# Optimization experiments

Measured on AMD Instinct MI355X. Metric: run time of the kernel, lower is better.

Reference implementation:

```python
import jax, jax.numpy as jnp
import numpy as np

NH, DK, DV = 16, 32, 16   # num_heads, d_k, d_v ; NH*DV == 256 (residual constraint)
CIN = 256
B, S = 4, 32
EPS = 1e-6


def setup_inputs() -> dict:
    key = jax.random.key(0)
    ks = jax.random.split(key, 16)
    def w(k, shape, fan_in):
        return jax.random.normal(k, shape, jnp.float32) / np.sqrt(fan_in)
    return {
        "x":  jax.random.normal(ks[0], (B, S, S, S, CIN), jnp.float32),
        "Wq": w(ks[1], (CIN, NH * DK), CIN), "bq": jnp.zeros((NH * DK,), jnp.float32),
        "Wk": w(ks[2], (CIN, NH * DK), CIN), "bk": jnp.zeros((NH * DK,), jnp.float32),
        "Wv": w(ks[3], (CIN, NH * DV), CIN), "bv": jnp.zeros((NH * DV,), jnp.float32),
        "W1": w(ks[4], (NH * DV, 2 * NH * DK), NH * DV), "b1": jnp.zeros((2 * NH * DK,), jnp.float32),
        "Wo": w(ks[5], (2 * NH * DK, NH * DV), 2 * NH * DK), "bo": jnp.zeros((NH * DV,), jnp.float32),
        "Wc": w(ks[6], (CIN, 256), CIN), "bc": jnp.zeros((256,), jnp.float32),
        "gamma": jnp.ones((256,), jnp.float32),
        "beta": jnp.zeros((256,), jnp.float32),
        "mu": jnp.zeros((256,), jnp.float32),
        "var": jnp.ones((256,), jnp.float32),
    }


def reference(x, Wq, bq, Wk, bk, Wv, bv, W1, b1, Wo, bo, Wc, bc, gamma, beta, mu, var):
    # 1x1x1 convs == per-voxel dense projections over the channel axis
    q = x @ Wq + bq                                  # [B,S,S,S,NH*DK]
    k = x @ Wk + bk
    v = x @ Wv + bv
    n = B * S * S * S
    q = q.reshape(n, NH, DK)
    k = k.reshape(n, NH, DK)
    v = v.reshape(n, NH, DV)
    # per-voxel attention among heads: scores [n, NH, NH]
    scores = jnp.einsum('nhd,ngd->nhg', q, k) / jnp.sqrt(jnp.float32(DK))
    attn = jax.nn.softmax(scores, axis=-1)
    attn_out = jnp.einsum('nhg,ngv->nhv', attn, v)   # [n, NH, DV]
    attn_out = attn_out.reshape(B, S, S, S, NH * DV)
    # conv FFN
    inter = jax.nn.relu(attn_out @ W1 + b1)          # [B,S,S,S,2*NH*DK]
    inter = inter @ Wo + bo                          # [B,S,S,S,NH*DV]
    # residual branch: 1x1 conv to 256 channels with relu
    res = jax.nn.relu(x @ Wc + bc)                   # [B,S,S,S,256]
    # inference-mode batchnorm (epsilon=1e-6)
    y = (res + inter - mu) * jax.lax.rsqrt(var + EPS) * gamma + beta
    return y
```

## Files before the change

### kernel.cpp

```cpp
#include <hip/hip_runtime.h>
#include <hip/hip_bf16.h>


typedef __bf16 bf16;
typedef __bf16 bf16x8 __attribute__((ext_vector_type(8)));
typedef float f32x4 __attribute__((ext_vector_type(4)));

#define MFMA(a, b, c) __builtin_amdgcn_mfma_f32_16x16x32_bf16((a), (b), (c), 0, 0, 0)

#define THREADS 512
#define TILE 32

constexpr int CIN = 256, NQK = 512, NV = 256, NI = 1024;

constexpr int CH_WQ = 0;
constexpr int CH_WK = 16384;
constexpr int CH_WV = 32768;
constexpr int CH_W1 = 40960;
constexpr int CH_WO = 73728;
constexpr int CH_WC = 106496;
constexpr int CH_TOT = 114688;

constexpr int L_XF  = 0;
constexpr int L_AOF = 8192;
constexpr int L_C   = 16384;
constexpr int L_QS  = L_C;
constexpr int L_KS  = L_C + 16896;
constexpr int L_VS  = L_C + 33792;
constexpr int L_INTF = L_C;
constexpr int LDS_ELEMS = 16384 + 42496;

__global__ void pack_w(const float* __restrict__ Wq, const float* __restrict__ Wk,
                       const float* __restrict__ Wv, const float* __restrict__ W1,
                       const float* __restrict__ Wo, const float* __restrict__ Wc,
                       bf16* __restrict__ ws) {
    int c = blockIdx.x * 256 + threadIdx.x;
    if (c >= CH_TOT) return;
    const float* W; int N, KT, lc;
    if (c < CH_WK)      { W = Wq; N = 512;  KT = 8;  lc = c - CH_WQ; }
    else if (c < CH_WV) { W = Wk; N = 512;  KT = 8;  lc = c - CH_WK; }
    else if (c < CH_W1) { W = Wv; N = 256;  KT = 8;  lc = c - CH_WV; }
    else if (c < CH_WO) { W = W1; N = 1024; KT = 8;  lc = c - CH_W1; }
    else if (c < CH_WC) { W = Wo; N = 256;  KT = 32; lc = c - CH_WO; }
    else                { W = Wc; N = 256;  KT = 8;  lc = c - CH_WC; }
    int lane = lc & 63, tmp = lc >> 6;
    int kt = tmp % KT, nt = tmp / KT;
    int k0 = kt * 32 + (lane >> 4) * 8;
    int n  = nt * 16 + (lane & 15);
    bf16x8 v;
    #pragma unroll
    for (int j = 0; j < 8; ++j) v[j] = (bf16)W[(size_t)(k0 + j) * N + n];
    *(bf16x8*)(ws + (size_t)c * 8) = v;
}

__device__ __forceinline__ bf16x8 lds_afrag(const bf16* smb, int baseoff, int KT,
                                            int mt, int kt, int lane) {
    return *(const bf16x8*)(smb + baseoff + (((mt * KT + kt) * 64) + lane) * 8);
}

__global__ __launch_bounds__(THREADS)
void msa_mfma(const float* __restrict__ x, const bf16* __restrict__ ws,
              const float* __restrict__ bq, const float* __restrict__ bk,
              const float* __restrict__ bv, const float* __restrict__ b1,
              const float* __restrict__ bo, const float* __restrict__ bc,
              const float* __restrict__ gamma, const float* __restrict__ beta,
              const float* __restrict__ mu, const float* __restrict__ var,
              float* __restrict__ out)
{
    extern __shared__ bf16 smb[];
    const int t = threadIdx.x;
    const int lane = t & 63;
    const int wave = t >> 6;
    const int col = lane & 15;
    const int qd  = lane >> 4;
    const size_t base = (size_t)blockIdx.x * (TILE * CIN);

    #pragma unroll
    for (int c2 = t; c2 < 1024; c2 += THREADS) {
        int lc = c2 & 63, kt = (c2 >> 6) & 7, mt = c2 >> 9;
        int vox = mt * 16 + (lc & 15);
        int k0  = kt * 32 + (lc >> 4) * 8;
        const float* src = x + base + vox * 256 + k0;
        float4 f0 = *(const float4*)src;
        float4 f1 = *(const float4*)(src + 4);
        bf16x8 h;
        h[0] = (bf16)f0.x; h[1] = (bf16)f0.y; h[2] = (bf16)f0.z; h[3] = (bf16)f0.w;
        h[4] = (bf16)f1.x; h[5] = (bf16)f1.y; h[6] = (bf16)f1.z; h[7] = (bf16)f1.w;
        *(bf16x8*)&smb[L_XF + c2 * 8] = h;
    }
    __syncthreads();

    {
        f32x4 acc[10][2];
        #pragma unroll
        for (int i = 0; i < 10; ++i) {
            acc[i][0] = (f32x4){0.f, 0.f, 0.f, 0.f};
            acc[i][1] = (f32x4){0.f, 0.f, 0.f, 0.f};
        }
        const bf16* wbase[10];
        #pragma unroll
        for (int i = 0; i < 10; ++i) {
            int g = wave * 10 + i;
            int ch;
            if (g < 32)      ch = CH_WQ + g * 512;
            else if (g < 64) ch = CH_WK + (g - 32) * 512;
            else             ch = CH_WV + (g - 64) * 512;
            wbase[i] = ws + ((size_t)ch + lane) * 8;
        }
        for (int kt = 0; kt < 8; ++kt) {
            bf16x8 a0 = lds_afrag(smb, L_XF, 8, 0, kt, lane);
            bf16x8 a1 = lds_afrag(smb, L_XF, 8, 1, kt, lane);
            #pragma unroll
            for (int i = 0; i < 10; ++i) {
                bf16x8 b = *(const bf16x8*)(wbase[i] + kt * 512);
                acc[i][0] = MFMA(a0, b, acc[i][0]);
                acc[i][1] = MFMA(a1, b, acc[i][1]);
            }
        }
        #pragma unroll
        for (int i = 0; i < 10; ++i) {
            int g = wave * 10 + i;
            int plane, stride, chan;
            float bias;
            if (g < 32)      { chan = g * 16 + col;        bias = bq[chan]; plane = L_QS; stride = 528; }
            else if (g < 64) { chan = (g - 32) * 16 + col; bias = bk[chan]; plane = L_KS; stride = 528; }
            else             { chan = (g - 64) * 16 + col; bias = bv[chan]; plane = L_VS; stride = 272; }
            #pragma unroll
            for (int mt = 0; mt < 2; ++mt)
                #pragma unroll
                for (int r = 0; r < 4; ++r) {
                    int vox = mt * 16 + qd * 4 + r;
                    smb[plane + vox * stride + chan] = (bf16)(acc[i][mt][r] + bias);
                }
        }
    }
    __syncthreads();

    {
        const int vox = t >> 4, h = t & 15;
        const bf16* qp = smb + L_QS + vox * 528 + h * 32;
        float qf[32];
        #pragma unroll
        for (int d8 = 0; d8 < 4; ++d8) {
            bf16x8 qv = *(const bf16x8*)(qp + d8 * 8);
            #pragma unroll
            for (int j = 0; j < 8; ++j) qf[d8 * 8 + j] = (float)qv[j];
        }
        float sc_[16];
        #pragma unroll
        for (int g = 0; g < 16; ++g) {
            const bf16* kp = smb + L_KS + vox * 528 + g * 32;
            float s = 0.f;
            #pragma unroll
            for (int d8 = 0; d8 < 4; ++d8) {
                bf16x8 kv = *(const bf16x8*)(kp + d8 * 8);
                #pragma unroll
                for (int j = 0; j < 8; ++j) s = fmaf((float)kv[j], qf[d8 * 8 + j], s);
            }
            sc_[g] = s * 0.17677669529663687f;
        }
        float m = sc_[0];
        #pragma unroll
        for (int g = 1; g < 16; ++g) m = fmaxf(m, sc_[g]);
        float sum = 0.f;
        #pragma unroll
        for (int g = 0; g < 16; ++g) { sc_[g] = __expf(sc_[g] - m); sum += sc_[g]; }
        const float inv = 1.f / sum;
        float ao[16];
        #pragma unroll
        for (int j = 0; j < 16; ++j) ao[j] = 0.f;
        #pragma unroll
        for (int g = 0; g < 16; ++g) {
            const float a = sc_[g];
            const bf16* vp = smb + L_VS + vox * 272 + g * 16;
            #pragma unroll
            for (int v8 = 0; v8 < 2; ++v8) {
                bf16x8 vv = *(const bf16x8*)(vp + v8 * 8);
                #pragma unroll
                for (int j = 0; j < 8; ++j)
                    ao[v8 * 8 + j] = fmaf(a, (float)vv[j], ao[v8 * 8 + j]);
            }
        }
        const int mt = vox >> 4, m_ = vox & 15, kt = h >> 1;
        #pragma unroll
        for (int half = 0; half < 2; ++half) {
            int quad = (h & 1) * 2 + half;
            bf16x8 o;
            #pragma unroll
            for (int j = 0; j < 8; ++j) o[j] = (bf16)(ao[half * 8 + j] * inv);
            *(bf16x8*)&smb[L_AOF + (((mt * 8 + kt) * 64) + quad * 16 + m_) * 8] = o;
        }
    }
    __syncthreads();

    {
        f32x4 acc[8][2];
        #pragma unroll
        for (int i = 0; i < 8; ++i) {
            acc[i][0] = (f32x4){0.f, 0.f, 0.f, 0.f};
            acc[i][1] = (f32x4){0.f, 0.f, 0.f, 0.f};
        }
        const int n0 = wave * 8;
        for (int kt = 0; kt < 8; ++kt) {
            bf16x8 a0 = lds_afrag(smb, L_AOF, 8, 0, kt, lane);
            bf16x8 a1 = lds_afrag(smb, L_AOF, 8, 1, kt, lane);
            #pragma unroll
            for (int i = 0; i < 8; ++i) {
                bf16x8 b = *(const bf16x8*)(ws + ((size_t)(CH_W1 + ((n0 + i) * 8 + kt) * 64) + lane) * 8);
                acc[i][0] = MFMA(a0, b, acc[i][0]);
                acc[i][1] = MFMA(a1, b, acc[i][1]);
            }
        }
        __syncthreads();
        #pragma unroll
        for (int i = 0; i < 8; ++i) {
            int c = (n0 + i) * 16 + col;
            float bias = b1[c];
            int kt2 = c >> 5;
            int q2  = (c & 31) >> 3;
            int j2  = c & 7;
            #pragma unroll
            for (int mt = 0; mt < 2; ++mt)
                #pragma unroll
                for (int r = 0; r < 4; ++r) {
                    int m_ = qd * 4 + r;
                    float v = fmaxf(acc[i][mt][r] + bias, 0.f);
                    smb[L_INTF + (((mt * 32 + kt2) * 64) + q2 * 16 + m_) * 8 + j2] = (bf16)v;
                }
        }
    }
    __syncthreads();

    {
        f32x4 accF[2][2], accW[2][2];
        #pragma unroll
        for (int i = 0; i < 2; ++i)
            #pragma unroll
            for (int mt = 0; mt < 2; ++mt) {
                accF[i][mt] = (f32x4){0.f, 0.f, 0.f, 0.f};
                accW[i][mt] = (f32x4){0.f, 0.f, 0.f, 0.f};
            }
        const int n0 = wave * 2;
        for (int kt = 0; kt < 32; ++kt) {
            bf16x8 a0 = lds_afrag(smb, L_INTF, 32, 0, kt, lane);
            bf16x8 a1 = lds_afrag(smb, L_INTF, 32, 1, kt, lane);
            #pragma unroll
            for (int i = 0; i < 2; ++i) {
                bf16x8 b = *(const bf16x8*)(ws + ((size_t)(CH_WO + ((n0 + i) * 32 + kt) * 64) + lane) * 8);
                accF[i][0] = MFMA(a0, b, accF[i][0]);
                accF[i][1] = MFMA(a1, b, accF[i][1]);
            }
        }
        for (int kt = 0; kt < 8; ++kt) {
            bf16x8 a0 = lds_afrag(smb, L_XF, 8, 0, kt, lane);
            bf16x8 a1 = lds_afrag(smb, L_XF, 8, 1, kt, lane);
            #pragma unroll
            for (int i = 0; i < 2; ++i) {
                bf16x8 b = *(const bf16x8*)(ws + ((size_t)(CH_WC + ((n0 + i) * 8 + kt) * 64) + lane) * 8);
                accW[i][0] = MFMA(a0, b, accW[i][0]);
                accW[i][1] = MFMA(a1, b, accW[i][1]);
            }
        }
        #pragma unroll
        for (int i = 0; i < 2; ++i) {
            int c = (n0 + i) * 16 + col;
            float bo_ = bo[c], bc_ = bc[c];
            float scl = gamma[c] * rsqrtf(var[c] + 1e-6f);
            float mu_ = mu[c], be_ = beta[c];
            #pragma unroll
            for (int mt = 0; mt < 2; ++mt)
                #pragma unroll
                for (int r = 0; r < 4; ++r) {
                    int vox = mt * 16 + qd * 4 + r;
                    float res = fmaxf(accW[i][mt][r] + bc_, 0.f);
                    float iv  = accF[i][mt][r] + bo_;
                    out[base + vox * 256 + c] = (res + iv - mu_) * scl + be_;
                }
        }
    }
}

extern "C" void kernel_launch(void* const* d_in, const int* in_sizes, int n_in,
                              void* d_out, int out_size, void* d_ws, size_t ws_size,
                              hipStream_t stream) {
    const float* x     = (const float*)d_in[0];
    const float* Wq    = (const float*)d_in[1];
    const float* bq    = (const float*)d_in[2];
    const float* Wk    = (const float*)d_in[3];
    const float* bk    = (const float*)d_in[4];
    const float* Wv    = (const float*)d_in[5];
    const float* bv    = (const float*)d_in[6];
    const float* W1    = (const float*)d_in[7];
    const float* b1    = (const float*)d_in[8];
    const float* Wo    = (const float*)d_in[9];
    const float* bo    = (const float*)d_in[10];
    const float* Wc    = (const float*)d_in[11];
    const float* bc    = (const float*)d_in[12];
    const float* gamma = (const float*)d_in[13];
    const float* beta  = (const float*)d_in[14];
    const float* mu    = (const float*)d_in[15];
    const float* var   = (const float*)d_in[16];
    float* out = (float*)d_out;
    bf16* ws = (bf16*)d_ws;

    pack_w<<<(CH_TOT + 255) / 256, 256, 0, stream>>>(Wq, Wk, Wv, W1, Wo, Wc, ws);

    const int n = in_sizes[0] / CIN;
    const int blocks = n / TILE;
    const size_t smem = LDS_ELEMS * sizeof(bf16);
    hipFuncSetAttribute(reinterpret_cast<const void*>(msa_mfma),
                        hipFuncAttributeMaxDynamicSharedMemorySize, (int)smem);
    msa_mfma<<<blocks, THREADS, smem, stream>>>(x, ws, bq, bk, bv, b1, bo, bc,
                                                gamma, beta, mu, var, out);
}
```

Before: 667.6 us.

## Double threads per block and split every stage across twice as many waves

Raises the block size from 512 to 1024 threads and halves each wave's share of work in the QKV, W1 and Wo/Wc GEMM stages. The per-voxel head attention is now split across thread pairs, combining max, sum and outputs with lane shuffles. A redundant barrier in the W1 stage is removed, and launch bounds ask for at least 4 waves per SIMD, which caps registers per thread. The aim is to hide latency better when only one block fits per CU because of LDS use; the cost is extra shuffles and less reuse of each A fragment per wave.

```diff
diff --git a/kernel.cpp b/kernel.cpp
--- a/kernel.cpp
+++ b/kernel.cpp
@@ -8,10 +8,10 @@
 
 #define MFMA(a, b, c) __builtin_amdgcn_mfma_f32_16x16x32_bf16((a), (b), (c), 0, 0, 0)
 
-#define THREADS 512
+#define THREADS 1024
 #define TILE 32
 
-constexpr int CIN = 256, NQK = 512, NV = 256, NI = 1024;
+constexpr int CIN = 256;
 
 constexpr int CH_WQ = 0;
 constexpr int CH_WK = 16384;
@@ -58,7 +58,7 @@
     return *(const bf16x8*)(smb + baseoff + (((mt * KT + kt) * 64) + lane) * 8);
 }
 
-__global__ __launch_bounds__(THREADS)
+__global__ __launch_bounds__(THREADS, 4)
 void msa_mfma(const float* __restrict__ x, const bf16* __restrict__ ws,
               const float* __restrict__ bq, const float* __restrict__ bk,
               const float* __restrict__ bv, const float* __restrict__ b1,
@@ -75,8 +75,8 @@
     const int qd  = lane >> 4;
     const size_t base = (size_t)blockIdx.x * (TILE * CIN);
 
-    #pragma unroll
-    for (int c2 = t; c2 < 1024; c2 += THREADS) {
+    {
+        int c2 = t;
         int lc = c2 & 63, kt = (c2 >> 6) & 7, mt = c2 >> 9;
         int vox = mt * 16 + (lc & 15);
         int k0  = kt * 32 + (lc >> 4) * 8;
@@ -91,16 +91,16 @@
     __syncthreads();
 
     {
-        f32x4 acc[10][2];
-        #pragma unroll
-        for (int i = 0; i < 10; ++i) {
+        f32x4 acc[5][2];
+        #pragma unroll
+        for (int i = 0; i < 5; ++i) {
             acc[i][0] = (f32x4){0.f, 0.f, 0.f, 0.f};
             acc[i][1] = (f32x4){0.f, 0.f, 0.f, 0.f};
         }
-        const bf16* wbase[10];
-        #pragma unroll
-        for (int i = 0; i < 10; ++i) {
-            int g = wave * 10 + i;
+        const bf16* wbase[5];
+        #pragma unroll
+        for (int i = 0; i < 5; ++i) {
+            int g = wave * 5 + i;
             int ch;
             if (g < 32)      ch = CH_WQ + g * 512;
             else if (g < 64) ch = CH_WK + (g - 32) * 512;
@@ -111,15 +111,15 @@
             bf16x8 a0 = lds_afrag(smb, L_XF, 8, 0, kt, lane);
             bf16x8 a1 = lds_afrag(smb, L_XF, 8, 1, kt, lane);
             #pragma unroll
-            for (int i = 0; i < 10; ++i) {
+            for (int i = 0; i < 5; ++i) {
                 bf16x8 b = *(const bf16x8*)(wbase[i] + kt * 512);
                 acc[i][0] = MFMA(a0, b, acc[i][0]);
                 acc[i][1] = MFMA(a1, b, acc[i][1]);
             }
         }
         #pragma unroll
-        for (int i = 0; i < 10; ++i) {
-            int g = wave * 10 + i;
+        for (int i = 0; i < 5; ++i) {
+            int g = wave * 5 + i;
             int plane, stride, chan;
             float bias;
             if (g < 32)      { chan = g * 16 + col;        bias = bq[chan]; plane = L_QS; stride = 528; }
@@ -137,7 +137,9 @@
     __syncthreads();
 
     {
-        const int vox = t >> 4, h = t & 15;
+        const int half = t & 1;
+        const int h   = (t >> 1) & 15;
+        const int vox = t >> 5;
         const bf16* qp = smb + L_QS + vox * 528 + h * 32;
         float qf[32];
         #pragma unroll
@@ -146,10 +148,10 @@
             #pragma unroll
             for (int j = 0; j < 8; ++j) qf[d8 * 8 + j] = (float)qv[j];
         }
-        float sc_[16];
-        #pragma unroll
-        for (int g = 0; g < 16; ++g) {
-            const bf16* kp = smb + L_KS + vox * 528 + g * 32;
+        float sc_[8];
+        #pragma unroll
+        for (int gg = 0; gg < 8; ++gg) {
+            const bf16* kp = smb + L_KS + vox * 528 + (half * 8 + gg) * 32;
             float s = 0.f;
             #pragma unroll
             for (int d8 = 0; d8 < 4; ++d8) {
@@ -157,22 +159,24 @@
                 #pragma unroll
                 for (int j = 0; j < 8; ++j) s = fmaf((float)kv[j], qf[d8 * 8 + j], s);
             }
-            sc_[g] = s * 0.17677669529663687f;
+            sc_[gg] = s * 0.17677669529663687f;
         }
         float m = sc_[0];
         #pragma unroll
-        for (int g = 1; g < 16; ++g) m = fmaxf(m, sc_[g]);
+        for (int gg = 1; gg < 8; ++gg) m = fmaxf(m, sc_[gg]);
+        m = fmaxf(m, __shfl_xor(m, 1));
         float sum = 0.f;
         #pragma unroll
-        for (int g = 0; g < 16; ++g) { sc_[g] = __expf(sc_[g] - m); sum += sc_[g]; }
+        for (int gg = 0; gg < 8; ++gg) { sc_[gg] = __expf(sc_[gg] - m); sum += sc_[gg]; }
+        sum += __shfl_xor(sum, 1);
         const float inv = 1.f / sum;
         float ao[16];
         #pragma unroll
         for (int j = 0; j < 16; ++j) ao[j] = 0.f;
         #pragma unroll
-        for (int g = 0; g < 16; ++g) {
-            const float a = sc_[g];
-            const bf16* vp = smb + L_VS + vox * 272 + g * 16;
+        for (int gg = 0; gg < 8; ++gg) {
+            const float a = sc_[gg];
+            const bf16* vp = smb + L_VS + vox * 272 + (half * 8 + gg) * 16;
             #pragma unroll
             for (int v8 = 0; v8 < 2; ++v8) {
                 bf16x8 vv = *(const bf16x8*)(vp + v8 * 8);
@@ -181,39 +185,37 @@
                     ao[v8 * 8 + j] = fmaf(a, (float)vv[j], ao[v8 * 8 + j]);
             }
         }
+        #pragma unroll
+        for (int j = 0; j < 16; ++j) ao[j] += __shfl_xor(ao[j], 1);
         const int mt = vox >> 4, m_ = vox & 15, kt = h >> 1;
-        #pragma unroll
-        for (int half = 0; half < 2; ++half) {
-            int quad = (h & 1) * 2 + half;
-            bf16x8 o;
-            #pragma unroll
-            for (int j = 0; j < 8; ++j) o[j] = (bf16)(ao[half * 8 + j] * inv);
-            *(bf16x8*)&smb[L_AOF + (((mt * 8 + kt) * 64) + quad * 16 + m_) * 8] = o;
-        }
+        const int quad = (h & 1) * 2 + half;
+        bf16x8 o;
+        #pragma unroll
+        for (int j = 0; j < 8; ++j) o[j] = (bf16)(ao[half * 8 + j] * inv);
+        *(bf16x8*)&smb[L_AOF + (((mt * 8 + kt) * 64) + quad * 16 + m_) * 8] = o;
     }
     __syncthreads();
 
     {
-        f32x4 acc[8][2];
-        #pragma unroll
-        for (int i = 0; i < 8; ++i) {
+        f32x4 acc[4][2];
+        #pragma unroll
+        for (int i = 0; i < 4; ++i) {
             acc[i][0] = (f32x4){0.f, 0.f, 0.f, 0.f};
             acc[i][1] = (f32x4){0.f, 0.f, 0.f, 0.f};
         }
-        const int n0 = wave * 8;
+        const int n0 = wave * 4;
         for (int kt = 0; kt < 8; ++kt) {
             bf16x8 a0 = lds_afrag(smb, L_AOF, 8, 0, kt, lane);
             bf16x8 a1 = lds_afrag(smb, L_AOF, 8, 1, kt, lane);
             #pragma unroll
-            for (int i = 0; i < 8; ++i) {
+            for (int i = 0; i < 4; ++i) {
                 bf16x8 b = *(const bf16x8*)(ws + ((size_t)(CH_W1 + ((n0 + i) * 8 + kt) * 64) + lane) * 8);
                 acc[i][0] = MFMA(a0, b, acc[i][0]);
                 acc[i][1] = MFMA(a1, b, acc[i][1]);
             }
         }
-        __syncthreads();
-        #pragma unroll
-        for (int i = 0; i < 8; ++i) {
+        #pragma unroll
+        for (int i = 0; i < 4; ++i) {
             int c = (n0 + i) * 16 + col;
             float bias = b1[c];
             int kt2 = c >> 5;
@@ -232,38 +234,28 @@
     __syncthreads();
 
     {
-        f32x4 accF[2][2], accW[2][2];
-        #pragma unroll
-        for (int i = 0; i < 2; ++i)
-            #pragma unroll
-            for (int mt = 0; mt < 2; ++mt) {
-                accF[i][mt] = (f32x4){0.f, 0.f, 0.f, 0.f};
-                accW[i][mt] = (f32x4){0.f, 0.f, 0.f, 0.f};
-            }
-        const int n0 = wave * 2;
+        f32x4 accF[2], accW[2];
+        accF[0] = (f32x4){0.f, 0.f, 0.f, 0.f};
+        accF[1] = (f32x4){0.f, 0.f, 0.f, 0.f};
+        accW[0] = (f32x4){0.f, 0.f, 0.f, 0.f};
+        accW[1] = (f32x4){0.f, 0.f, 0.f, 0.f};
+        const int n0 = wave;
         for (int kt = 0; kt < 32; ++kt) {
             bf16x8 a0 = lds_afrag(smb, L_INTF, 32, 0, kt, lane);
             bf16x8 a1 = lds_afrag(smb, L_INTF, 32, 1, kt, lane);
-            #pragma unroll
-            for (int i = 0; i < 2; ++i) {
-                bf16x8 b = *(const bf16x8*)(ws + ((size_t)(CH_WO + ((n0 + i) * 32 + kt) * 64) + lane) * 8);
-                accF[i][0] = MFMA(a0, b, accF[i][0]);
-                accF[i][1] = MFMA(a1, b, accF[i][1]);
-            }
+            bf16x8 b = *(const bf16x8*)(ws + ((size_t)(CH_WO + (n0 * 32 + kt) * 64) + lane) * 8);
+            accF[0] = MFMA(a0, b, accF[0]);
+            accF[1] = MFMA(a1, b, accF[1]);
         }
         for (int kt = 0; kt < 8; ++kt) {
             bf16x8 a0 = lds_afrag(smb, L_XF, 8, 0, kt, lane);
             bf16x8 a1 = lds_afrag(smb, L_XF, 8, 1, kt, lane);
-            #pragma unroll
-            for (int i = 0; i < 2; ++i) {
-                bf16x8 b = *(const bf16x8*)(ws + ((size_t)(CH_WC + ((n0 + i) * 8 + kt) * 64) + lane) * 8);
-                accW[i][0] = MFMA(a0, b, accW[i][0]);
-                accW[i][1] = MFMA(a1, b, accW[i][1]);
-            }
-        }
-        #pragma unroll
-        for (int i = 0; i < 2; ++i) {
-            int c = (n0 + i) * 16 + col;
+            bf16x8 b = *(const bf16x8*)(ws + ((size_t)(CH_WC + (n0 * 8 + kt) * 64) + lane) * 8);
+            accW[0] = MFMA(a0, b, accW[0]);
+            accW[1] = MFMA(a1, b, accW[1]);
+        }
+        {
+            int c = n0 * 16 + col;
             float bo_ = bo[c], bc_ = bc[c];
             float scl = gamma[c] * rsqrtf(var[c] + 1e-6f);
             float mu_ = mu[c], be_ = beta[c];
@@ -272,8 +264,8 @@
                 #pragma unroll
                 for (int r = 0; r < 4; ++r) {
                     int vox = mt * 16 + qd * 4 + r;
-                    float res = fmaxf(accW[i][mt][r] + bc_, 0.f);
-                    float iv  = accF[i][mt][r] + bo_;
+                    float res = fmaxf(accW[mt][r] + bc_, 0.f);
+                    float iv  = accF[mt][r] + bo_;
                     out[base + vox * 256 + c] = (res + iv - mu_) * scl + be_;
                 }
         }
```

After: 706.5 us. 5.8% more time.
